# Performance work log

Measured on AMD Instinct MI355X. Metric: run time of the kernel, lower is better.

## Reference

```python
import jax, jax.numpy as jnp
import numpy as np

N = 262144   # query points
M = 131072   # gather-source points
C = 256      # c1 == c2
H = C // 8   # gating bottleneck
EPS = 1e-5


def _bn(x, g, b):
    # BatchNorm1d in training mode: biased batch stats over the point dim.
    mu = jnp.mean(x, axis=0)
    var = jnp.mean((x - mu) ** 2, axis=0)
    return (x - mu) * jax.lax.rsqrt(var + EPS) * g + b


def setup_inputs() -> dict:
    key = jax.random.key(0)
    ks = jax.random.split(key, 8)
    p = jax.random.normal(ks[0], (N, 3), dtype=jnp.float32)
    x = jax.random.normal(ks[1], (N, C), dtype=jnp.float32)
    gx = jax.random.normal(ks[2], (M, C), dtype=jnp.float32)
    idx = jax.random.randint(ks[3], (N,), 0, M, dtype=jnp.int64)
    s = 0.05
    return {
        "p": p, "x": x, "gx": gx, "idx": idx,
        # nn.Linear(c1, c1, bias=False)
        "Wlin": jax.random.normal(ks[4], (C, C), dtype=jnp.float32) * s,
        # self.bn
        "g_main": jnp.ones((C,), jnp.float32), "b_main": jnp.zeros((C,), jnp.float32),
        # linear_w: BN(c2) -> Linear(c2, c2//8) -> BN(c2//8) -> Linear(c2//8, c2)
        "g_a": jnp.ones((C,), jnp.float32), "b_a": jnp.zeros((C,), jnp.float32),
        "W1": jax.random.normal(ks[5], (H, C), dtype=jnp.float32) * s,
        "b1": jnp.zeros((H,), jnp.float32),
        "g_b": jnp.ones((H,), jnp.float32), "b_b": jnp.zeros((H,), jnp.float32),
        "W2": jax.random.normal(ks[6], (C, H), dtype=jnp.float32) * s,
        "b2": jnp.zeros((C,), jnp.float32),
    }


def reference(p, x, gx, idx, Wlin, g_main, b_main, g_a, b_a, W1, b1, g_b, b_b, W2, b2):
    # kNN(k=1) gather: aug_feat = gx[idx]
    aug = gx[idx]                                    # (N, C)
    # relation '-' with c1 == c2
    rel = x - aug                                    # (N, C)
    # linear_w gating MLP
    rel = jax.nn.relu(_bn(rel, g_a, b_a))
    rel = rel @ W1.T + b1                            # (N, H)
    rel = jax.nn.relu(_bn(rel, g_b, b_b))
    rel = rel @ W2.T + b2                            # (N, C)
    sw = jax.nn.softmax(rel, axis=1)
    # residual combine (c1 == c2 branch), then Linear -> BN -> ReLU
    x2 = x + sw * aug                                # (N, C)
    out = jax.nn.relu(_bn(x2 @ Wlin.T, g_main, b_main))
    return out  # p, o are passed through unchanged by the module
```

## Files before the change

kernel.cpp:

```cpp
#include <hip/hip_runtime.h>
#include <stdint.h>
#include <stddef.h>

#define N_PTS 262144
#define M_PTS 131072
#define C_DIM 256
#define H_DIM 32
#define EPS_BN 1e-5f
#define NSLOT_A 64
#define NSLOT_B 16
#define NSLOT_T 64

using s16x8 = __attribute__((ext_vector_type(8))) short;
using s16x4 = __attribute__((ext_vector_type(4))) short;
using f32x4 = __attribute__((ext_vector_type(4))) float;

__device__ __forceinline__ short f2bf(float f) {
  __bf16 h = (__bf16)f;
  return __builtin_bit_cast(short, h);
}
__device__ __forceinline__ float bf2f(short s) {
  unsigned int u = ((unsigned int)(unsigned short)s) << 16;
  return __builtin_bit_cast(float, u);
}
__device__ __forceinline__ f32x4 mfma16(s16x8 a, s16x8 b, f32x4 c) {
  return __builtin_amdgcn_mfma_f32_16x16x32_bf16(a, b, c, 0, 0, 0);
}

__global__ __launch_bounds__(256) void k_prep(
    const float* __restrict__ W1, const float* __restrict__ W2,
    const float* __restrict__ Wlin, short* __restrict__ W1b,
    short* __restrict__ W2b, short* __restrict__ Wlb) {
  int i = blockIdx.x * 256 + threadIdx.x;
  if (i < 8192) {
    W1b[i] = f2bf(W1[i]);
  } else if (i < 16384) {
    W2b[i - 8192] = f2bf(W2[i - 8192]);
  } else {
    int s = i - 16384;
    int col = s >> 8, k = s & 255;
    int ks = k >> 6, kf = k & 63;
    Wlb[ks * 16384 + col * 64 + kf] = f2bf(Wlin[s]);
  }
}

__global__ __launch_bounds__(256) void k_rel(
    const float* __restrict__ x, const float* __restrict__ gx,
    const int* __restrict__ idx, short* __restrict__ rel,
    float* __restrict__ sum_a) {
  __shared__ float red[4][512];
  int t = threadIdx.x;
  int w = t >> 6;
  int c4 = (t & 63) * 4;
  int r0 = blockIdx.x * 128;
  float s0 = 0, s1 = 0, s2 = 0, s3 = 0, q0 = 0, q1 = 0, q2 = 0, q3 = 0;
#pragma unroll 4
  for (int it = 0; it < 32; ++it) {
    int r = r0 + it * 4 + w;
    int ir = idx[r];
    float4 xv = *(const float4*)(x + (size_t)r * 256 + c4);
    float4 gv = *(const float4*)(gx + (size_t)ir * 256 + c4);
    float d0 = xv.x - gv.x, d1 = xv.y - gv.y, d2 = xv.z - gv.z, d3 = xv.w - gv.w;
    s16x4 h;
    h[0] = f2bf(d0); h[1] = f2bf(d1); h[2] = f2bf(d2); h[3] = f2bf(d3);
    *(s16x4*)(rel + (size_t)r * 256 + c4) = h;
    s0 += d0; s1 += d1; s2 += d2; s3 += d3;
    q0 += d0 * d0; q1 += d1 * d1; q2 += d2 * d2; q3 += d3 * d3;
  }
  red[w][c4 + 0] = s0; red[w][c4 + 1] = s1; red[w][c4 + 2] = s2; red[w][c4 + 3] = s3;
  red[w][256 + c4 + 0] = q0; red[w][256 + c4 + 1] = q1;
  red[w][256 + c4 + 2] = q2; red[w][256 + c4 + 3] = q3;
  __syncthreads();
  float vs = red[0][t] + red[1][t] + red[2][t] + red[3][t];
  float vq = red[0][256 + t] + red[1][256 + t] + red[2][256 + t] + red[3][256 + t];
  float* slot = sum_a + (size_t)(blockIdx.x & (NSLOT_A - 1)) * 512;
  atomicAdd(&slot[t], vs);
  atomicAdd(&slot[256 + t], vq);
}

__global__ void k_fin(const float* __restrict__ sums, const float* __restrict__ g,
                      const float* __restrict__ b, float* __restrict__ sc,
                      float* __restrict__ sh, int n, float invN, int nslot) {
  int c = threadIdx.x;
  if (c < n) {
    float S = 0.f, Q = 0.f;
    for (int s = 0; s < nslot; ++s) {
      S += sums[(size_t)s * 2 * n + c];
      Q += sums[(size_t)s * 2 * n + n + c];
    }
    float mu = S * invN;
    float var = Q * invN - mu * mu;
    float rs = rsqrtf(var + EPS_BN);
    float scale = g[c] * rs;
    sc[c] = scale;
    sh[c] = b[c] - mu * scale;
  }
}

__global__ __launch_bounds__(256) void k_y(
    const short* __restrict__ rel, const short* __restrict__ W1b,
    const float* __restrict__ sc_a, const float* __restrict__ sh_a,
    short* __restrict__ yh, float* __restrict__ sum_b) {
  __shared__ __attribute__((aligned(16))) short Ab[64 * 264];
  __shared__ float lsc[256];
  __shared__ float lsh[256];
  __shared__ float red[4][64];
  int t = threadIdx.x;
  lsc[t] = sc_a[t];
  lsh[t] = sh_a[t];
  {
    int srow = t >> 2, sseg = (t & 3) * 64;
    const short* src = rel + (size_t)(blockIdx.x * 64 + srow) * 256 + sseg;
    short* dst = Ab + srow * 264 + sseg;
#pragma unroll
    for (int j = 0; j < 8; ++j)
      *(s16x8*)(dst + j * 8) = *(const s16x8*)(src + j * 8);
  }
  __syncthreads();
  int w = t >> 6, l = t & 63, l15 = l & 15, kg = l >> 4;
  int r0 = blockIdx.x * 64 + w * 16;
  const short* arow = Ab + (w * 16 + l15) * 264;

  s16x8 bfr[2][8];
#pragma unroll
  for (int j = 0; j < 2; ++j)
#pragma unroll
    for (int kk = 0; kk < 8; ++kk)
      bfr[j][kk] = *(const s16x8*)(W1b + (j * 16 + l15) * 256 + kg * 8 + kk * 32);

  f32x4 acc0 = {0.f, 0.f, 0.f, 0.f};
  f32x4 acc1 = {0.f, 0.f, 0.f, 0.f};
#pragma unroll
  for (int kk = 0; kk < 8; ++kk) {
    int k0 = kg * 8 + kk * 32;
    s16x8 a = *(const s16x8*)(arow + k0);
    s16x8 af;
#pragma unroll
    for (int i = 0; i < 8; ++i) {
      float v = bf2f(a[i]);
      v = fmaxf(v * lsc[k0 + i] + lsh[k0 + i], 0.f);
      af[i] = f2bf(v);
    }
    acc0 = mfma16(af, bfr[0][kk], acc0);
    acc1 = mfma16(af, bfr[1][kk], acc1);
  }

  float s0 = 0.f, q0 = 0.f, s1 = 0.f, q1 = 0.f;
#pragma unroll
  for (int reg = 0; reg < 4; ++reg) {
    int gr = r0 + kg * 4 + reg;
    float y0 = acc0[reg], y1 = acc1[reg];
    yh[(size_t)gr * 32 + l15] = f2bf(y0);
    yh[(size_t)gr * 32 + 16 + l15] = f2bf(y1);
    s0 += y0; q0 += y0 * y0;
    s1 += y1; q1 += y1 * y1;
  }
  s0 += __shfl_xor(s0, 16); s0 += __shfl_xor(s0, 32);
  q0 += __shfl_xor(q0, 16); q0 += __shfl_xor(q0, 32);
  s1 += __shfl_xor(s1, 16); s1 += __shfl_xor(s1, 32);
  q1 += __shfl_xor(q1, 16); q1 += __shfl_xor(q1, 32);
  if (l < 16) {
    red[w][l15] = s0;
    red[w][16 + l15] = s1;
    red[w][32 + l15] = q0;
    red[w][48 + l15] = q1;
  }
  __syncthreads();
  if (t < 64) {
    float v = red[0][t] + red[1][t] + red[2][t] + red[3][t];
    atomicAdd(&sum_b[(size_t)(blockIdx.x & (NSLOT_B - 1)) * 64 + t], v);
  }
}

__global__ __launch_bounds__(256) void k_x2(
    const short* __restrict__ yh, const short* __restrict__ W2b,
    const float* __restrict__ b2, const float* __restrict__ x,
    const float* __restrict__ sc_b, const float* __restrict__ sh_b,
    short* __restrict__ relx2) {
  __shared__ __attribute__((aligned(16))) short swl[64 * 264];
  int t = threadIdx.x, w = t >> 6, l = t & 63, l15 = l & 15, kg = l >> 4;
  int r0 = blockIdx.x * 64 + w * 16;
  int lr = r0 + l15;

  s16x8 yb = *(const s16x8*)(yh + (size_t)lr * 32 + kg * 8);
  s16x8 af;
#pragma unroll
  for (int i = 0; i < 8; ++i) {
    int k = kg * 8 + i;
    float v = bf2f(yb[i]);
    v = fmaxf(v * sc_b[k] + sh_b[k], 0.f);
    af[i] = f2bf(v);
  }

  f32x4 zero = {0.f, 0.f, 0.f, 0.f};
  f32x4 z[16];
#pragma unroll
  for (int n = 0; n < 16; ++n) {
    s16x8 bf = *(const s16x8*)(W2b + (n * 16 + l15) * 32 + kg * 8);
    z[n] = mfma16(af, bf, zero);
  }

  float b2c[16];
#pragma unroll
  for (int n = 0; n < 16; ++n) b2c[n] = b2[n * 16 + l15];

  float mx[4] = {-3.4e38f, -3.4e38f, -3.4e38f, -3.4e38f};
#pragma unroll
  for (int n = 0; n < 16; ++n)
#pragma unroll
    for (int r = 0; r < 4; ++r) {
      z[n][r] += b2c[n];
      mx[r] = fmaxf(mx[r], z[n][r]);
    }
#pragma unroll
  for (int r = 0; r < 4; ++r) {
    mx[r] = fmaxf(mx[r], __shfl_xor(mx[r], 1));
    mx[r] = fmaxf(mx[r], __shfl_xor(mx[r], 2));
    mx[r] = fmaxf(mx[r], __shfl_xor(mx[r], 4));
    mx[r] = fmaxf(mx[r], __shfl_xor(mx[r], 8));
  }
  float sm[4] = {0.f, 0.f, 0.f, 0.f};
#pragma unroll
  for (int n = 0; n < 16; ++n)
#pragma unroll
    for (int r = 0; r < 4; ++r) {
      float e = __expf(z[n][r] - mx[r]);
      z[n][r] = e;
      sm[r] += e;
    }
#pragma unroll
  for (int r = 0; r < 4; ++r) {
    sm[r] += __shfl_xor(sm[r], 1);
    sm[r] += __shfl_xor(sm[r], 2);
    sm[r] += __shfl_xor(sm[r], 4);
    sm[r] += __shfl_xor(sm[r], 8);
    sm[r] = 1.f / sm[r];
  }

#pragma unroll
  for (int n = 0; n < 16; ++n)
#pragma unroll
    for (int r = 0; r < 4; ++r)
      swl[(w * 16 + kg * 4 + r) * 264 + n * 16 + l15] = f2bf(z[n][r] * sm[r]);
  __syncthreads();

  int brow0 = blockIdx.x * 64;
  int c4 = (t & 63) * 4;
#pragma unroll 4
  for (int it = 0; it < 16; ++it) {
    int row = it * 4 + w;
    size_t goff = (size_t)(brow0 + row) * 256 + c4;
    float4 xv = *(const float4*)(x + goff);
    s16x4 rv = *(const s16x4*)(relx2 + goff);
    s16x4 sv = *(const s16x4*)(swl + row * 264 + c4);
    s16x4 h;
#pragma unroll
    for (int j = 0; j < 4; ++j) {
      float xf = xv[j];
      float aug = xf - bf2f(rv[j]);
      h[j] = f2bf(xf + bf2f(sv[j]) * aug);
    }
    *(s16x4*)(relx2 + goff) = h;
  }
}

__global__ __launch_bounds__(256) void k_gemm_t(
    short* __restrict__ x2t, const short* __restrict__ Wlb,
    float* __restrict__ sum_t) {
  __shared__ __attribute__((aligned(16))) short Ab[64 * 264];
  __shared__ __attribute__((aligned(16))) short Bb[256 * 72];
  __shared__ float ls[512];
  int t = threadIdx.x;
  {
    int srow = t >> 2, sseg = (t & 3) * 64;
    const short* src = x2t + (size_t)(blockIdx.x * 64 + srow) * 256 + sseg;
    short* dst = Ab + srow * 264 + sseg;
#pragma unroll
    for (int j = 0; j < 8; ++j)
      *(s16x8*)(dst + j * 8) = *(const s16x8*)(src + j * 8);
  }
  int w = t >> 6, l = t & 63, l15 = l & 15, kg = l >> 4;
  f32x4 zero = {0.f, 0.f, 0.f, 0.f};
  f32x4 acc[16];
#pragma unroll
  for (int n = 0; n < 16; ++n) acc[n] = zero;

  for (int ks = 0; ks < 4; ++ks) {
    __syncthreads();
#pragma unroll
    for (int j = 0; j < 8; ++j) {
      int u = j * 256 + t;
      *(s16x8*)(Bb + (u >> 3) * 72 + (u & 7) * 8) =
          *(const s16x8*)(Wlb + ks * 16384 + u * 8);
    }
    __syncthreads();
#pragma unroll
    for (int kk = 0; kk < 2; ++kk) {
      s16x8 a = *(const s16x8*)(Ab + (w * 16 + l15) * 264 + ks * 64 + kk * 32 + kg * 8);
#pragma unroll
      for (int n = 0; n < 16; ++n) {
        s16x8 b = *(const s16x8*)(Bb + (n * 16 + l15) * 72 + kk * 32 + kg * 8);
        acc[n] = mfma16(a, b, acc[n]);
      }
    }
  }

  ls[t] = 0.f;
  ls[256 + t] = 0.f;
  __syncthreads();
#pragma unroll
  for (int n = 0; n < 16; ++n) {
    float sY = acc[n][0] + acc[n][1] + acc[n][2] + acc[n][3];
    float sQ = acc[n][0] * acc[n][0] + acc[n][1] * acc[n][1] +
               acc[n][2] * acc[n][2] + acc[n][3] * acc[n][3];
    sY += __shfl_xor(sY, 16); sY += __shfl_xor(sY, 32);
    sQ += __shfl_xor(sQ, 16); sQ += __shfl_xor(sQ, 32);
    if (l < 16) {
      atomicAdd(&ls[n * 16 + l15], sY);
      atomicAdd(&ls[256 + n * 16 + l15], sQ);
    }
  }
  __syncthreads();
  float* slot = sum_t + (size_t)(blockIdx.x & (NSLOT_T - 1)) * 512;
  atomicAdd(&slot[t], ls[t]);
  atomicAdd(&slot[256 + t], ls[256 + t]);

#pragma unroll
  for (int n = 0; n < 16; ++n) {
#pragma unroll
    for (int r = 0; r < 4; ++r) {
      int gr = blockIdx.x * 64 + w * 16 + kg * 4 + r;
      x2t[(size_t)gr * 256 + n * 16 + l15] = f2bf(acc[n][r]);
    }
  }
}

__global__ __launch_bounds__(256) void k_out(
    const short* __restrict__ tbuf, const float* __restrict__ sc_m,
    const float* __restrict__ sh_m, float* __restrict__ out) {
  __shared__ float lsc[256];
  __shared__ float lsh[256];
  int t = threadIdx.x;
  lsc[t] = sc_m[t];
  lsh[t] = sh_m[t];
  __syncthreads();
  int u0 = blockIdx.x * 256 + t;
#pragma unroll 4
  for (int it = 0; it < 16; ++it) {
    int u = u0 + it * (2048 * 256);
    int c8 = (u & 31) * 8;
    s16x8 tv = *(const s16x8*)(tbuf + (size_t)u * 8);
    float4 sca = *(const float4*)(lsc + c8);
    float4 scb = *(const float4*)(lsc + c8 + 4);
    float4 sha = *(const float4*)(lsh + c8);
    float4 shb = *(const float4*)(lsh + c8 + 4);
    float4 o0, o1;
    o0.x = fmaxf(bf2f(tv[0]) * sca.x + sha.x, 0.f);
    o0.y = fmaxf(bf2f(tv[1]) * sca.y + sha.y, 0.f);
    o0.z = fmaxf(bf2f(tv[2]) * sca.z + sha.z, 0.f);
    o0.w = fmaxf(bf2f(tv[3]) * sca.w + sha.w, 0.f);
    o1.x = fmaxf(bf2f(tv[4]) * scb.x + shb.x, 0.f);
    o1.y = fmaxf(bf2f(tv[5]) * scb.y + shb.y, 0.f);
    o1.z = fmaxf(bf2f(tv[6]) * scb.z + shb.z, 0.f);
    o1.w = fmaxf(bf2f(tv[7]) * scb.w + shb.w, 0.f);
    *(float4*)(out + (size_t)u * 8) = o0;
    *(float4*)(out + (size_t)u * 8 + 4) = o1;
  }
}

extern "C" void kernel_launch(void* const* d_in, const int* in_sizes, int n_in,
                              void* d_out, int out_size, void* d_ws, size_t ws_size,
                              hipStream_t stream) {
  const float* x      = (const float*)d_in[1];
  const float* gx     = (const float*)d_in[2];
  const int*   idx    = (const int*)d_in[3];
  const float* Wlin   = (const float*)d_in[4];
  const float* g_main = (const float*)d_in[5];
  const float* b_main = (const float*)d_in[6];
  const float* g_a    = (const float*)d_in[7];
  const float* b_a    = (const float*)d_in[8];
  const float* W1     = (const float*)d_in[9];
  const float* g_b    = (const float*)d_in[11];
  const float* b_b    = (const float*)d_in[12];
  const float* W2     = (const float*)d_in[13];
  const float* b2     = (const float*)d_in[14];
  float* out = (float*)d_out;
  float* wsf = (float*)d_ws;

  float* sum_b = wsf;
  float* sc_a = wsf + 1024; float* sh_a = wsf + 1280;
  float* sc_b = wsf + 1536; float* sh_b = wsf + 1568;
  float* sc_m = wsf + 1600; float* sh_m = wsf + 1856;
  short* W1b = (short*)(wsf + 2112);
  short* W2b = (short*)(wsf + 6208);
  short* Wlb = (short*)(wsf + 10304);

  size_t big_off = (ws_size - (size_t)134217728) & ~(size_t)1023;
  size_t yh_off  = big_off - (size_t)16777216;
  short* big = (short*)((char*)d_ws + big_off);
  short* yh  = (short*)((char*)d_ws + yh_off);
  float* sum_a = (float*)((char*)d_ws + yh_off);
  float* sum_t = sum_a;

  hipMemsetAsync(sum_b, 0, 1024 * sizeof(float), stream);
  hipMemsetAsync(sum_a, 0, 32768 * sizeof(float), stream);
  k_prep<<<320, 256, 0, stream>>>(W1, W2, Wlin, W1b, W2b, Wlb);
  k_rel<<<N_PTS / 128, 256, 0, stream>>>(x, gx, idx, big, sum_a);
  k_fin<<<1, 256, 0, stream>>>(sum_a, g_a, b_a, sc_a, sh_a, 256, 1.f / N_PTS, NSLOT_A);
  k_y<<<N_PTS / 64, 256, 0, stream>>>(big, W1b, sc_a, sh_a, yh, sum_b);
  k_fin<<<1, 64, 0, stream>>>(sum_b, g_b, b_b, sc_b, sh_b, 32, 1.f / N_PTS, NSLOT_B);
  k_x2<<<N_PTS / 64, 256, 0, stream>>>(yh, W2b, b2, x, sc_b, sh_b, big);
  hipMemsetAsync(sum_t, 0, 32768 * sizeof(float), stream);
  k_gemm_t<<<N_PTS / 64, 256, 0, stream>>>(big, Wlb, sum_t);
  k_fin<<<1, 256, 0, stream>>>(sum_t, g_main, b_main, sc_m, sh_m, 256, 1.f / N_PTS, NSLOT_T);
  k_out<<<2048, 256, 0, stream>>>(big, sc_m, sh_m, out);
}
```

Baseline: 572.1 us.

## Fuse residual combine with final Linear GEMM, stream pre-swizzled weights from global

Merges k_x2 and k_gemm_t into one kernel. The combined x2 tile stays in shared memory and feeds the Linear MFMA directly, which removes a full bf16 write and re-read of the N×256 intermediate and one kernel launch. Wlin is pre-swizzled into an MFMA fragment layout so each lane loads B fragments straight from global/L2 with no shared-memory staging or barriers. BN stat scratch moves into the tail of the output buffer, which gets overwritten later by k_out. The costs are higher register pressure in the fused kernel and every block re-reading the 128KB weight from cache.

```diff
diff --git a/kernel.cpp b/kernel.cpp
--- a/kernel.cpp
+++ b/kernel.cpp
@@ -30,7 +30,7 @@
 __global__ __launch_bounds__(256) void k_prep(
     const float* __restrict__ W1, const float* __restrict__ W2,
     const float* __restrict__ Wlin, short* __restrict__ W1b,
-    short* __restrict__ W2b, short* __restrict__ Wlb) {
+    short* __restrict__ W2b, short* __restrict__ Wlb2) {
   int i = blockIdx.x * 256 + threadIdx.x;
   if (i < 8192) {
     W1b[i] = f2bf(W1[i]);
@@ -39,8 +39,9 @@
   } else {
     int s = i - 16384;
     int col = s >> 8, k = s & 255;
-    int ks = k >> 6, kf = k & 63;
-    Wlb[ks * 16384 + col * 64 + kf] = f2bf(Wlin[s]);
+    int ksl = k >> 5, kg = (k >> 3) & 3, e = k & 7;
+    int n = col >> 4, cl = col & 15;
+    Wlb2[(((ksl * 16 + n) * 4 + kg) * 16 + cl) * 8 + e] = f2bf(Wlin[s]);
   }
 }
 
@@ -172,12 +173,14 @@
   }
 }
 
-__global__ __launch_bounds__(256) void k_x2(
+__global__ __launch_bounds__(256) void k_x2g(
     const short* __restrict__ yh, const short* __restrict__ W2b,
     const float* __restrict__ b2, const float* __restrict__ x,
-    const float* __restrict__ sc_b, const float* __restrict__ sh_b,
-    short* __restrict__ relx2) {
+    const short* __restrict__ Wlb2, const float* __restrict__ sc_b,
+    const float* __restrict__ sh_b, short* __restrict__ big,
+    float* __restrict__ sum_t) {
   __shared__ __attribute__((aligned(16))) short swl[64 * 264];
+  __shared__ float ls[512];
   int t = threadIdx.x, w = t >> 6, l = t & 63, l15 = l & 15, kg = l >> 4;
   int r0 = blockIdx.x * 64 + w * 16;
   int lr = r0 + l15;
@@ -191,7 +194,6 @@
     v = fmaxf(v * sc_b[k] + sh_b[k], 0.f);
     af[i] = f2bf(v);
   }
-
   f32x4 zero = {0.f, 0.f, 0.f, 0.f};
   f32x4 z[16];
 #pragma unroll
@@ -199,11 +201,9 @@
     s16x8 bf = *(const s16x8*)(W2b + (n * 16 + l15) * 32 + kg * 8);
     z[n] = mfma16(af, bf, zero);
   }
-
   float b2c[16];
 #pragma unroll
   for (int n = 0; n < 16; ++n) b2c[n] = b2[n * 16 + l15];
-
   float mx[4] = {-3.4e38f, -3.4e38f, -3.4e38f, -3.4e38f};
 #pragma unroll
   for (int n = 0; n < 16; ++n)
@@ -236,7 +236,6 @@
     sm[r] += __shfl_xor(sm[r], 8);
     sm[r] = 1.f / sm[r];
   }
-
 #pragma unroll
   for (int n = 0; n < 16; ++n)
 #pragma unroll
@@ -251,7 +250,7 @@
     int row = it * 4 + w;
     size_t goff = (size_t)(brow0 + row) * 256 + c4;
     float4 xv = *(const float4*)(x + goff);
-    s16x4 rv = *(const s16x4*)(relx2 + goff);
+    s16x4 rv = *(const s16x4*)(big + goff);
     s16x4 sv = *(const s16x4*)(swl + row * 264 + c4);
     s16x4 h;
 #pragma unroll
@@ -260,48 +259,20 @@
       float aug = xf - bf2f(rv[j]);
       h[j] = f2bf(xf + bf2f(sv[j]) * aug);
     }
-    *(s16x4*)(relx2 + goff) = h;
-  }
-}
-
-__global__ __launch_bounds__(256) void k_gemm_t(
-    short* __restrict__ x2t, const short* __restrict__ Wlb,
-    float* __restrict__ sum_t) {
-  __shared__ __attribute__((aligned(16))) short Ab[64 * 264];
-  __shared__ __attribute__((aligned(16))) short Bb[256 * 72];
-  __shared__ float ls[512];
-  int t = threadIdx.x;
-  {
-    int srow = t >> 2, sseg = (t & 3) * 64;
-    const short* src = x2t + (size_t)(blockIdx.x * 64 + srow) * 256 + sseg;
-    short* dst = Ab + srow * 264 + sseg;
-#pragma unroll
-    for (int j = 0; j < 8; ++j)
-      *(s16x8*)(dst + j * 8) = *(const s16x8*)(src + j * 8);
-  }
-  int w = t >> 6, l = t & 63, l15 = l & 15, kg = l >> 4;
-  f32x4 zero = {0.f, 0.f, 0.f, 0.f};
+    *(s16x4*)(swl + row * 264 + c4) = h;
+  }
+  __syncthreads();
+
   f32x4 acc[16];
 #pragma unroll
   for (int n = 0; n < 16; ++n) acc[n] = zero;
-
-  for (int ks = 0; ks < 4; ++ks) {
-    __syncthreads();
-#pragma unroll
-    for (int j = 0; j < 8; ++j) {
-      int u = j * 256 + t;
-      *(s16x8*)(Bb + (u >> 3) * 72 + (u & 7) * 8) =
-          *(const s16x8*)(Wlb + ks * 16384 + u * 8);
-    }
-    __syncthreads();
-#pragma unroll
-    for (int kk = 0; kk < 2; ++kk) {
-      s16x8 a = *(const s16x8*)(Ab + (w * 16 + l15) * 264 + ks * 64 + kk * 32 + kg * 8);
-#pragma unroll
-      for (int n = 0; n < 16; ++n) {
-        s16x8 b = *(const s16x8*)(Bb + (n * 16 + l15) * 72 + kk * 32 + kg * 8);
-        acc[n] = mfma16(a, b, acc[n]);
-      }
+#pragma unroll
+  for (int ksl = 0; ksl < 8; ++ksl) {
+    s16x8 a = *(const s16x8*)(swl + (w * 16 + l15) * 264 + ksl * 32 + kg * 8);
+#pragma unroll
+    for (int n = 0; n < 16; ++n) {
+      s16x8 b = *(const s16x8*)(Wlb2 + (((size_t)ksl * 16 + n) * 64 + l) * 8);
+      acc[n] = mfma16(a, b, acc[n]);
     }
   }
 
@@ -329,8 +300,8 @@
   for (int n = 0; n < 16; ++n) {
 #pragma unroll
     for (int r = 0; r < 4; ++r) {
-      int gr = blockIdx.x * 64 + w * 16 + kg * 4 + r;
-      x2t[(size_t)gr * 256 + n * 16 + l15] = f2bf(acc[n][r]);
+      int gr = brow0 + w * 16 + kg * 4 + r;
+      big[(size_t)gr * 256 + n * 16 + l15] = f2bf(acc[n][r]);
     }
   }
 }
@@ -391,27 +362,26 @@
   float* sc_a = wsf + 1024; float* sh_a = wsf + 1280;
   float* sc_b = wsf + 1536; float* sh_b = wsf + 1568;
   float* sc_m = wsf + 1600; float* sh_m = wsf + 1856;
-  short* W1b = (short*)(wsf + 2112);
-  short* W2b = (short*)(wsf + 6208);
-  short* Wlb = (short*)(wsf + 10304);
+  short* W1b  = (short*)(wsf + 2112);
+  short* W2b  = (short*)(wsf + 6208);
+  short* Wlb2 = (short*)(wsf + 10304);
 
   size_t big_off = (ws_size - (size_t)134217728) & ~(size_t)1023;
   size_t yh_off  = big_off - (size_t)16777216;
   short* big = (short*)((char*)d_ws + big_off);
   short* yh  = (short*)((char*)d_ws + yh_off);
-  float* sum_a = (float*)((char*)d_ws + yh_off);
-  float* sum_t = sum_a;
+
+  float* sum_t = out + (size_t)N_PTS * 256 - 65536;
+  float* sum_a = out + (size_t)N_PTS * 256 - 32768;
 
   hipMemsetAsync(sum_b, 0, 1024 * sizeof(float), stream);
-  hipMemsetAsync(sum_a, 0, 32768 * sizeof(float), stream);
-  k_prep<<<320, 256, 0, stream>>>(W1, W2, Wlin, W1b, W2b, Wlb);
+  hipMemsetAsync(sum_t, 0, 65536 * sizeof(float), stream);
+  k_prep<<<320, 256, 0, stream>>>(W1, W2, Wlin, W1b, W2b, Wlb2);
   k_rel<<<N_PTS / 128, 256, 0, stream>>>(x, gx, idx, big, sum_a);
   k_fin<<<1, 256, 0, stream>>>(sum_a, g_a, b_a, sc_a, sh_a, 256, 1.f / N_PTS, NSLOT_A);
   k_y<<<N_PTS / 64, 256, 0, stream>>>(big, W1b, sc_a, sh_a, yh, sum_b);
   k_fin<<<1, 64, 0, stream>>>(sum_b, g_b, b_b, sc_b, sh_b, 32, 1.f / N_PTS, NSLOT_B);
-  k_x2<<<N_PTS / 64, 256, 0, stream>>>(yh, W2b, b2, x, sc_b, sh_b, big);
-  hipMemsetAsync(sum_t, 0, 32768 * sizeof(float), stream);
-  k_gemm_t<<<N_PTS / 64, 256, 0, stream>>>(big, Wlb, sum_t);
+  k_x2g<<<N_PTS / 64, 256, 0, stream>>>(yh, W2b, b2, x, Wlb2, sc_b, sh_b, big, sum_t);
   k_fin<<<1, 256, 0, stream>>>(sum_t, g_main, b_main, sc_m, sh_m, 256, 1.f / N_PTS, NSLOT_T);
   k_out<<<2048, 256, 0, stream>>>(big, sc_m, sh_m, out);
 }
```

After: 609.2 us. +6.5%, slower.
